# Kernel optimization log

Hardware: AMD Instinct MI355X
Metric: run time of the kernel (lower is better)

## Reference

```python
import jax, jax.numpy as jnp
import numpy as np

BS, H, W, C = 32, 64, 64, 256
SEQ = 32


def setup_inputs() -> dict:
    key = jax.random.key(0)
    k1, k2, k3, k4, k5 = jax.random.split(key, 5)
    x = jax.random.normal(k1, (BS, H, W, C), dtype=jnp.float32)
    sentence = jax.random.normal(k2, (BS, C), dtype=jnp.float32)  # unused in call()
    context = jax.random.normal(k3, (BS, SEQ, C), dtype=jnp.float32)
    mask = jax.random.bernoulli(k4, 0.3, (BS, SEQ))
    W_word = jax.random.normal(k5, (C, C), dtype=jnp.float32) * (1.0 / np.sqrt(C))
    return {"x": x, "sentence": sentence, "context": context, "mask": mask, "W_word": W_word}


def reference(x, sentence, context, mask, W_word):
    bs, h, w, c = x.shape
    hw = h * w
    seq = context.shape[1]
    xf = x.reshape(bs, hw, c)                                   # [bs, hw, C]
    ctx = jnp.einsum('bsd,dc->bsc', context, W_word)            # conv1x1 word projection
    attn = jnp.einsum('bnc,bsc->bns', xf, ctx)                  # [bs, hw, seq]
    attn = attn.reshape(bs * hw, seq)
    # faithful to original: mask tiled hw times along axis 0 (block-repeat order)
    mask_t = jnp.tile(mask, (hw, 1))                            # [bs*hw, seq]
    neg_inf = jnp.asarray(-jnp.inf, dtype=attn.dtype)
    attn = jnp.where(mask_t, neg_inf, attn)
    attn = jax.nn.softmax(attn, axis=-1).reshape(bs, hw, seq)
    # matmul(ctx^T, attn^T) -> [bs, C, hw] -> transpose -> [bs, hw, C]
    weighted_context = jnp.einsum('bsc,bns->bnc', ctx, attn).reshape(bs, h, w, c)
    word_attn = attn.reshape(bs, h, w, seq)
    return weighted_context, word_attn
```

## Files before the change

### kernel.cpp

```cpp
#include <hip/hip_runtime.h>
#include <stdint.h>

typedef __attribute__((ext_vector_type(8))) short short8;
typedef __attribute__((ext_vector_type(4))) float float4v;

#define HW   4096
#define CC   256
#define SEQQ 32
#define BSZ  32
#define ROWS 64
#define PSTR 48

static __device__ __forceinline__ uint16_t f2bf(float f) {
  union { float f; uint32_t u; } v; v.f = f;
  uint32_t r = v.u + 0x7FFFu + ((v.u >> 16) & 1u);
  return (uint16_t)(r >> 16);
}
static __device__ __forceinline__ float bf2f(uint16_t h) {
  union { uint32_t u; float f; } v; v.u = ((uint32_t)h) << 16;
  return v.f;
}

extern "C" __global__ __launch_bounds__(256) void prep_kernel(
    const float* __restrict__ ctx_in,
    const float* __restrict__ Wp,
    const void*  __restrict__ mask,
    float* __restrict__ bias_ws,
    uint16_t* __restrict__ ctx_hi_ws,
    uint16_t* __restrict__ ctx_lo_ws,
    uint16_t* __restrict__ ctxT_ws)
{
  const int t = threadIdx.x;
  if (blockIdx.x == 256) {
    __shared__ int byteFlag;
    if (t == 0) byteFlag = 0;
    __syncthreads();
    const uint8_t* mb = (const uint8_t*)mask;
    int nz = 0;
    for (int i = t; i < 1024; i += 256)
      if ((i & 3) == 1 && mb[i] != 0) nz = 1;
    if (nz) atomicOr(&byteFlag, 1);
    __syncthreads();
    const bool byteMode = (byteFlag != 0);
    const uint32_t* mw = (const uint32_t*)mask;
    for (int i = t; i < 1024; i += 256) {
      bool m = byteMode ? (mb[i] != 0) : (mw[i] != 0);
      bias_ws[i] = m ? -1e30f : 0.0f;
    }
    return;
  }

  const int r0 = blockIdx.x * 4;
  __shared__ float crow[4][CC];
  #pragma unroll
  for (int j = 0; j < 4; ++j)
    crow[j][t] = ctx_in[(size_t)(r0 + j) * CC + t];
  __syncthreads();

  float acc[4] = {0.f, 0.f, 0.f, 0.f};
  for (int d = 0; d < CC; ++d) {
    float wv = Wp[(size_t)d * CC + t];
    #pragma unroll
    for (int j = 0; j < 4; ++j) acc[j] += crow[j][d] * wv;
  }
  #pragma unroll
  for (int j = 0; j < 4; ++j) {
    int row = r0 + j;
    int bb = row >> 5, ss = row & 31;
    float v = acc[j];
    uint16_t h = f2bf(v);
    uint16_t lo = f2bf(v - bf2f(h));
    ctx_hi_ws[(size_t)row * CC + t] = h;
    ctx_lo_ws[(size_t)row * CC + t] = lo;
    ctxT_ws[((size_t)bb * CC + t) * SEQQ + ss] = h;
  }
}

extern "C" __global__ __launch_bounds__(256) void attn_main(
    const float* __restrict__ x,
    const uint8_t* __restrict__ ws,
    float* __restrict__ out0,
    float* __restrict__ out1)
{
  const float*    bias_ws   = (const float*)ws;
  const uint16_t* ctx_hi_ws = (const uint16_t*)(ws + 4096);
  const uint16_t* ctx_lo_ws = ctx_hi_ws + BSZ * SEQQ * CC;
  const uint16_t* ctxT_ws   = ctx_lo_ws + BSZ * SEQQ * CC;

  __shared__ __align__(16) uint16_t ctxHi[SEQQ * 264];
  __shared__ __align__(16) uint16_t ctxLo[SEQQ * 264];
  __shared__ __align__(16) uint16_t ctxT[CC * PSTR];
  __shared__ __align__(16) float    biasL[BSZ * SEQQ];
  __shared__ __align__(16) uint16_t pL[ROWS * PSTR];

  const int tid = threadIdx.x;
  const int b   = blockIdx.y;
  const int n0  = blockIdx.x * ROWS;

  {
    const uint4* s_hi = (const uint4*)(ctx_hi_ws + (size_t)b * SEQQ * CC);
    const uint4* s_lo = (const uint4*)(ctx_lo_ws + (size_t)b * SEQQ * CC);
    const uint4* s_T  = (const uint4*)(ctxT_ws  + (size_t)b * CC * SEQQ);
    for (int i = tid; i < 1024; i += 256) {
      int row = i >> 5, col = i & 31;
      *(uint4*)&ctxHi[row * 264 + col * 8] = s_hi[i];
      *(uint4*)&ctxLo[row * 264 + col * 8] = s_lo[i];
    }
    for (int i = tid; i < 1024; i += 256) {
      int c = i >> 2, col = i & 3;
      *(uint4*)&ctxT[c * PSTR + col * 8] = s_T[i];
    }
    ((uint4*)biasL)[tid] = ((const uint4*)bias_ws)[tid];
  }
  __syncthreads();

  const int w    = tid >> 6;
  const int lane = tid & 63;
  const int l15  = lane & 15;
  const int quad = lane >> 4;
  const int nbase = n0 + w * 16;

  float4v acc0 = {0.f, 0.f, 0.f, 0.f};
  float4v acc1 = {0.f, 0.f, 0.f, 0.f};
  const float* xrow = x + ((size_t)b * HW + nbase + l15) * CC + quad * 8;

  for (int k0 = 0; k0 < 8; ++k0) {
    float4 xa = *(const float4*)(xrow + k0 * 32);
    float4 xb = *(const float4*)(xrow + k0 * 32 + 4);
    float xv[8] = {xa.x, xa.y, xa.z, xa.w, xb.x, xb.y, xb.z, xb.w};
    short8 ah, al;
    #pragma unroll
    for (int j = 0; j < 8; ++j) {
      uint16_t h = f2bf(xv[j]);
      ah[j] = (short)h;
      al[j] = (short)f2bf(xv[j] - bf2f(h));
    }
    const int kb = k0 * 32 + quad * 8;
    short8 bh0 = *(const short8*)&ctxHi[l15 * 264 + kb];
    short8 bl0 = *(const short8*)&ctxLo[l15 * 264 + kb];
    short8 bh1 = *(const short8*)&ctxHi[(16 + l15) * 264 + kb];
    short8 bl1 = *(const short8*)&ctxLo[(16 + l15) * 264 + kb];
    acc0 = __builtin_amdgcn_mfma_f32_16x16x32_bf16(ah, bh0, acc0, 0, 0, 0);
    acc0 = __builtin_amdgcn_mfma_f32_16x16x32_bf16(ah, bl0, acc0, 0, 0, 0);
    acc0 = __builtin_amdgcn_mfma_f32_16x16x32_bf16(al, bh0, acc0, 0, 0, 0);
    acc1 = __builtin_amdgcn_mfma_f32_16x16x32_bf16(ah, bh1, acc1, 0, 0, 0);
    acc1 = __builtin_amdgcn_mfma_f32_16x16x32_bf16(ah, bl1, acc1, 0, 0, 0);
    acc1 = __builtin_amdgcn_mfma_f32_16x16x32_bf16(al, bh1, acc1, 0, 0, 0);
  }

  #pragma unroll
  for (int r = 0; r < 4; ++r) {
    const int n  = nbase + quad * 4 + r;
    const int br = n & 31;
    float v0 = acc0[r] + biasL[br * 32 + l15];
    float v1 = acc1[r] + biasL[br * 32 + 16 + l15];
    float mx = fmaxf(v0, v1);
    #pragma unroll
    for (int off = 1; off < 16; off <<= 1)
      mx = fmaxf(mx, __shfl_xor(mx, off, 64));
    float e0 = __expf(v0 - mx);
    float e1 = __expf(v1 - mx);
    float sm = e0 + e1;
    #pragma unroll
    for (int off = 1; off < 16; off <<= 1)
      sm += __shfl_xor(sm, off, 64);
    float inv = 1.0f / sm;
    float p0 = e0 * inv, p1 = e1 * inv;
    size_t o1 = ((size_t)b * HW + n) * SEQQ;
    out1[o1 + l15]      = p0;
    out1[o1 + 16 + l15] = p1;
    pL[(w * 16 + quad * 4 + r) * PSTR + l15]      = f2bf(p0);
    pL[(w * 16 + quad * 4 + r) * PSTR + 16 + l15] = f2bf(p1);
  }
  __syncthreads();

  short8 pa = *(const short8*)&pL[(w * 16 + l15) * PSTR + quad * 8];
  #pragma unroll
  for (int ct = 0; ct < 16; ++ct) {
    short8 bfr = *(const short8*)&ctxT[(ct * 16 + l15) * PSTR + quad * 8];
    float4v z = {0.f, 0.f, 0.f, 0.f};
    float4v d = __builtin_amdgcn_mfma_f32_16x16x32_bf16(pa, bfr, z, 0, 0, 0);
    #pragma unroll
    for (int r = 0; r < 4; ++r) {
      size_t o0 = ((size_t)b * HW + nbase + quad * 4 + r) * CC + ct * 16 + l15;
      out0[o0] = d[r];
    }
  }
}

extern "C" void kernel_launch(void* const* d_in, const int* in_sizes, int n_in,
                              void* d_out, int out_size, void* d_ws, size_t ws_size,
                              hipStream_t stream) {
  const float* x      = (const float*)d_in[0];
  const float* ctx_in = (const float*)d_in[2];
  const void*  mask   = d_in[3];
  const float* Wp     = (const float*)d_in[4];

  float* out0 = (float*)d_out;
  float* out1 = out0 + (size_t)BSZ * HW * CC;

  uint8_t*  ws        = (uint8_t*)d_ws;
  float*    bias_ws   = (float*)ws;
  uint16_t* ctx_hi_ws = (uint16_t*)(ws + 4096);
  uint16_t* ctx_lo_ws = ctx_hi_ws + BSZ * SEQQ * CC;
  uint16_t* ctxT_ws   = ctx_lo_ws + BSZ * SEQQ * CC;

  prep_kernel<<<257, 256, 0, stream>>>(ctx_in, Wp, mask, bias_ws,
                                       ctx_hi_ws, ctx_lo_ws, ctxT_ws);
  attn_main<<<dim3(HW / ROWS, BSZ), 256, 0, stream>>>(x, ws, out0, out1);
}
```

Baseline: 284.9 us.

## Pre-swizzle ctx into MFMA fragment layout and read operands directly from global

The prep kernel now writes the bf16 hi/lo context and its transpose already permuted into the per-lane MFMA fragment order. The main kernel then loads each B operand as one coalesced 16-byte read from global/L2 instead of staging ~50KB into LDS per block. This removes the shared-memory fill and its barrier and cuts LDS usage, and occupancy is requested at 5 blocks per CU. In exchange, operand and bias reads go through the cache hierarchy for every block rather than being reused from LDS.

```diff
diff --git a/kernel.cpp b/kernel.cpp
--- a/kernel.cpp
+++ b/kernel.cpp
@@ -26,9 +26,9 @@
     const float* __restrict__ Wp,
     const void*  __restrict__ mask,
     float* __restrict__ bias_ws,
-    uint16_t* __restrict__ ctx_hi_ws,
-    uint16_t* __restrict__ ctx_lo_ws,
-    uint16_t* __restrict__ ctxT_ws)
+    uint16_t* __restrict__ hiF_ws,
+    uint16_t* __restrict__ loF_ws,
+    uint16_t* __restrict__ tF_ws)
 {
   const int t = threadIdx.x;
   if (blockIdx.x == 256) {
@@ -63,56 +63,41 @@
     #pragma unroll
     for (int j = 0; j < 4; ++j) acc[j] += crow[j][d] * wv;
   }
+
+  const int c  = t;
+  const int k0 = c >> 5, qd = (c >> 3) & 3, jj = c & 7;
+  const int ct = c >> 4, l15c = c & 15;
   #pragma unroll
   for (int j = 0; j < 4; ++j) {
     int row = r0 + j;
-    int bb = row >> 5, ss = row & 31;
+    int b = row >> 5, s = row & 31;
     float v = acc[j];
-    uint16_t h = f2bf(v);
+    uint16_t h  = f2bf(v);
     uint16_t lo = f2bf(v - bf2f(h));
-    ctx_hi_ws[(size_t)row * CC + t] = h;
-    ctx_lo_ws[(size_t)row * CC + t] = lo;
-    ctxT_ws[((size_t)bb * CC + t) * SEQQ + ss] = h;
+    size_t i1 = ((((size_t)b * 8 + k0) * 2 + (s >> 4)) * 64 + qd * 16 + (s & 15)) * 8 + jj;
+    hiF_ws[i1] = h;
+    loF_ws[i1] = lo;
+    size_t i2 = (((size_t)b * 16 + ct) * 64 + (s >> 3) * 16 + l15c) * 8 + (s & 7);
+    tF_ws[i2] = h;
   }
 }
 
-extern "C" __global__ __launch_bounds__(256) void attn_main(
+extern "C" __global__ __launch_bounds__(256, 5) void attn_main(
     const float* __restrict__ x,
     const uint8_t* __restrict__ ws,
     float* __restrict__ out0,
     float* __restrict__ out1)
 {
-  const float*    bias_ws   = (const float*)ws;
-  const uint16_t* ctx_hi_ws = (const uint16_t*)(ws + 4096);
-  const uint16_t* ctx_lo_ws = ctx_hi_ws + BSZ * SEQQ * CC;
-  const uint16_t* ctxT_ws   = ctx_lo_ws + BSZ * SEQQ * CC;
+  const float*  bias_ws = (const float*)ws;
+  const short8* hiF = (const short8*)(ws + 4096);
+  const short8* loF = hiF + BSZ * 8 * 2 * 64;
+  const short8* tF  = loF + BSZ * 8 * 2 * 64;
 
-  __shared__ __align__(16) uint16_t ctxHi[SEQQ * 264];
-  __shared__ __align__(16) uint16_t ctxLo[SEQQ * 264];
-  __shared__ __align__(16) uint16_t ctxT[CC * PSTR];
-  __shared__ __align__(16) float    biasL[BSZ * SEQQ];
   __shared__ __align__(16) uint16_t pL[ROWS * PSTR];
 
   const int tid = threadIdx.x;
   const int b   = blockIdx.y;
   const int n0  = blockIdx.x * ROWS;
-
-  {
-    const uint4* s_hi = (const uint4*)(ctx_hi_ws + (size_t)b * SEQQ * CC);
-    const uint4* s_lo = (const uint4*)(ctx_lo_ws + (size_t)b * SEQQ * CC);
-    const uint4* s_T  = (const uint4*)(ctxT_ws  + (size_t)b * CC * SEQQ);
-    for (int i = tid; i < 1024; i += 256) {
-      int row = i >> 5, col = i & 31;
-      *(uint4*)&ctxHi[row * 264 + col * 8] = s_hi[i];
-      *(uint4*)&ctxLo[row * 264 + col * 8] = s_lo[i];
-    }
-    for (int i = tid; i < 1024; i += 256) {
-      int c = i >> 2, col = i & 3;
-      *(uint4*)&ctxT[c * PSTR + col * 8] = s_T[i];
-    }
-    ((uint4*)biasL)[tid] = ((const uint4*)bias_ws)[tid];
-  }
-  __syncthreads();
 
   const int w    = tid >> 6;
   const int lane = tid & 63;
@@ -122,11 +107,17 @@
 
   float4v acc0 = {0.f, 0.f, 0.f, 0.f};
   float4v acc1 = {0.f, 0.f, 0.f, 0.f};
-  const float* xrow = x + ((size_t)b * HW + nbase + l15) * CC + quad * 8;
+  const float*  xrow  = x + ((size_t)b * HW + nbase + l15) * CC + quad * 8;
+  const short8* hiF_b = hiF + (size_t)b * 16 * 64 + lane;
+  const short8* loF_b = loF + (size_t)b * 16 * 64 + lane;
 
   for (int k0 = 0; k0 < 8; ++k0) {
     float4 xa = *(const float4*)(xrow + k0 * 32);
     float4 xb = *(const float4*)(xrow + k0 * 32 + 4);
+    short8 bh0 = hiF_b[(k0 * 2 + 0) * 64];
+    short8 bl0 = loF_b[(k0 * 2 + 0) * 64];
+    short8 bh1 = hiF_b[(k0 * 2 + 1) * 64];
+    short8 bl1 = loF_b[(k0 * 2 + 1) * 64];
     float xv[8] = {xa.x, xa.y, xa.z, xa.w, xb.x, xb.y, xb.z, xb.w};
     short8 ah, al;
     #pragma unroll
@@ -135,11 +126,6 @@
       ah[j] = (short)h;
       al[j] = (short)f2bf(xv[j] - bf2f(h));
     }
-    const int kb = k0 * 32 + quad * 8;
-    short8 bh0 = *(const short8*)&ctxHi[l15 * 264 + kb];
-    short8 bl0 = *(const short8*)&ctxLo[l15 * 264 + kb];
-    short8 bh1 = *(const short8*)&ctxHi[(16 + l15) * 264 + kb];
-    short8 bl1 = *(const short8*)&ctxLo[(16 + l15) * 264 + kb];
     acc0 = __builtin_amdgcn_mfma_f32_16x16x32_bf16(ah, bh0, acc0, 0, 0, 0);
     acc0 = __builtin_amdgcn_mfma_f32_16x16x32_bf16(ah, bl0, acc0, 0, 0, 0);
     acc0 = __builtin_amdgcn_mfma_f32_16x16x32_bf16(al, bh0, acc0, 0, 0, 0);
@@ -152,8 +138,8 @@
   for (int r = 0; r < 4; ++r) {
     const int n  = nbase + quad * 4 + r;
     const int br = n & 31;
-    float v0 = acc0[r] + biasL[br * 32 + l15];
-    float v1 = acc1[r] + biasL[br * 32 + 16 + l15];
+    float v0 = acc0[r] + bias_ws[br * 32 + l15];
+    float v1 = acc1[r] + bias_ws[br * 32 + 16 + l15];
     float mx = fmaxf(v0, v1);
     #pragma unroll
     for (int off = 1; off < 16; off <<= 1)
@@ -175,9 +161,10 @@
   __syncthreads();
 
   short8 pa = *(const short8*)&pL[(w * 16 + l15) * PSTR + quad * 8];
-  #pragma unroll
+  const short8* tF_b = tF + (size_t)b * 16 * 64 + lane;
+  #pragma unroll 4
   for (int ct = 0; ct < 16; ++ct) {
-    short8 bfr = *(const short8*)&ctxT[(ct * 16 + l15) * PSTR + quad * 8];
+    short8 bfr = tF_b[ct * 64];
     float4v z = {0.f, 0.f, 0.f, 0.f};
     float4v d = __builtin_amdgcn_mfma_f32_16x16x32_bf16(pa, bfr, z, 0, 0, 0);
     #pragma unroll
@@ -199,13 +186,13 @@
   float* out0 = (float*)d_out;
   float* out1 = out0 + (size_t)BSZ * HW * CC;
 
-  uint8_t*  ws        = (uint8_t*)d_ws;
-  float*    bias_ws   = (float*)ws;
-  uint16_t* ctx_hi_ws = (uint16_t*)(ws + 4096);
-  uint16_t* ctx_lo_ws = ctx_hi_ws + BSZ * SEQQ * CC;
-  uint16_t* ctxT_ws   = ctx_lo_ws + BSZ * SEQQ * CC;
+  uint8_t*  ws     = (uint8_t*)d_ws;
+  float*    bias_ws = (float*)ws;
+  uint16_t* hiF_ws = (uint16_t*)(ws + 4096);
+  uint16_t* loF_ws = hiF_ws + BSZ * 8 * 2 * 64 * 8;
+  uint16_t* tF_ws  = loF_ws + BSZ * 8 * 2 * 64 * 8;
 
   prep_kernel<<<257, 256, 0, stream>>>(ctx_in, Wp, mask, bias_ws,
-                                       ctx_hi_ws, ctx_lo_ws, ctxT_ws);
+                                       hiF_ws, loF_ws, tF_ws);
   attn_main<<<dim3(HW / ROWS, BSZ), 256, 0, stream>>>(x, ws, out0, out1);
 }
```

Measured after the change: 285.5 us. About the same (+0.2%).
